# Performance work log

Hardware: AMD Instinct MI355X
Metric: run time of the kernel (lower is better)

Reference implementation:

```python
import jax, jax.numpy as jnp
import numpy as np

D = 128  # h_dim == in_dim

def _gat_layer(h, d, src, dst, n_dst, W, U, V, a):
    # h: [N_src, Din], d: [E, 1], src/dst: [E]
    z = h @ W.T          # [N_src, D]
    zi = h @ U.T         # [N_src, D]
    t = d @ V.T          # [E, 1]
    Dh = W.shape[0]
    # attn_fc on concat([z_src, z_dst, t]) split into three partial dots
    e = z[src] @ a[:Dh] + z[dst] @ a[Dh:2 * Dh] + t[:, 0] * a[2 * Dh]
    e = jax.nn.leaky_relu(e)  # [E]
    # segment softmax over incoming edges of each dst node
    m = jax.ops.segment_max(e, dst, num_segments=n_dst)
    ex = jnp.exp(e - m[dst])
    s = jax.ops.segment_sum(ex, dst, num_segments=n_dst)
    alpha = ex / s[dst]  # [E]
    zn = jax.ops.segment_sum(alpha[:, None] * z[src], dst, num_segments=n_dst)
    return jax.nn.relu(zi[:n_dst] + zn)


def setup_inputs() -> dict:
    key = jax.random.key(0)
    ks = jax.random.split(key, 16)
    N0, ND0, ND1 = 100000, 40000, 20000
    E0, E1 = 640000, 320000
    sc = 1.0 / np.sqrt(D)
    inp = {
        "attr": jax.random.normal(ks[0], (N0, D), jnp.float32),
        "d0": jax.random.normal(ks[1], (E0, 1), jnp.float32),
        "d1": jax.random.normal(ks[2], (E1, 1), jnp.float32),
        "src0": jax.random.randint(ks[3], (E0,), 0, N0, jnp.int32),
        "dst0": jax.random.randint(ks[4], (E0,), 0, ND0, jnp.int32),
        "src1": jax.random.randint(ks[5], (E1,), 0, ND0, jnp.int32),
        "dst1": jax.random.randint(ks[6], (E1,), 0, ND1, jnp.int32),
        "n_dst0": ND0,
        "n_dst1": ND1,
        "W0": jax.random.normal(ks[7], (D, D), jnp.float32) * sc,
        "U0": jax.random.normal(ks[8], (D, D), jnp.float32) * sc,
        "V0": jax.random.normal(ks[9], (1, 1), jnp.float32),
        "a0": jax.random.normal(ks[10], (2 * D + 1,), jnp.float32) * sc,
        "W1": jax.random.normal(ks[11], (D, D), jnp.float32) * sc,
        "U1": jax.random.normal(ks[12], (D, D), jnp.float32) * sc,
        "V1": jax.random.normal(ks[13], (1, 1), jnp.float32),
        "a1": jax.random.normal(ks[14], (2 * D + 1,), jnp.float32) * sc,
    }
    return inp


def reference(attr, d0, d1, W0, U0, V0, a0, W1, U1, V1, a1,
              src0, dst0, src1, dst1, n_dst0, n_dst1):
    h = _gat_layer(attr, d0, src0, dst0, n_dst0, W0, U0, V0, a0)
    h = _gat_layer(h, d1, src1, dst1, n_dst1, W1, U1, V1, a1)
    return h
```

## Files before the change

### kernel.cpp

```cpp
#include <hip/hip_runtime.h>
#include <math.h>


#define D 128

typedef __bf16 bf16x8 __attribute__((ext_vector_type(8)));
typedef float f32x4 __attribute__((ext_vector_type(4)));

static __device__ __forceinline__ float lrelu(float x) {
  return x >= 0.f ? x : 0.01f * x;
}
static __device__ __forceinline__ unsigned short f2bf(float v) {
  unsigned int u = __float_as_uint(v);
  u += 0x7fffu + ((u >> 16) & 1u);
  return (unsigned short)(u >> 16);
}
static __device__ __forceinline__ float bf2f(unsigned short b) {
  return __uint_as_float((unsigned int)b << 16);
}

static __device__ __forceinline__ float4 loadV4(const float* p) {
  return *(const float4*)p;
}
static __device__ __forceinline__ float4 loadV4(const unsigned short* p) {
  ushort4 t = *(const ushort4*)p;
  return make_float4(bf2f(t.x), bf2f(t.y), bf2f(t.z), bf2f(t.w));
}
static __device__ __forceinline__ void storeV4(float* p, float4 v) {
  *(float4*)p = v;
}
static __device__ __forceinline__ void storeV4(unsigned short* p, float4 v) {
  ushort4 t;
  t.x = f2bf(v.x);
  t.y = f2bf(v.y);
  t.z = f2bf(v.z);
  t.w = f2bf(v.w);
  *(ushort4*)p = t;
}
static __device__ __forceinline__ void storeZi(float* p, float v) { *p = v; }
static __device__ __forceinline__ void storeZi(unsigned short* p, float v) {
  *p = f2bf(v);
}

static __device__ __forceinline__ int swz(int row, int colb) {
  return row * 256 + (colb ^ ((row & 7) << 4));
}

__global__ __launch_bounds__(256) void cvt4_kernel(
    const float* __restrict__ s0, const float* __restrict__ s1,
    const float* __restrict__ s2, const float* __restrict__ s3,
    __bf16* __restrict__ dst) {
  int idx = blockIdx.x * 256 + threadIdx.x;
  const float* s = (idx < 16384) ? s0
                   : (idx < 32768) ? s1
                   : (idx < 49152) ? s2 : s3;
  dst[idx] = (__bf16)s[idx & 16383];
}

__global__ void zero_int_kernel(int* __restrict__ p, int n) {
  int i = blockIdx.x * 256 + threadIdx.x;
  if (i < n) p[i] = 0;
}

static __device__ __forceinline__ void stageA(const float* A, int rblk,
                                              int rlim, int t,
                                              unsigned char* ldsA) {
  const char* base = (const char*)A + (size_t)rblk * 512;
#pragma unroll
  for (int g = 0; g < 8; ++g) {
    int sb = g * 4096 + t * 16;
    float4 v = make_float4(0.f, 0.f, 0.f, 0.f);
    if (rblk + (sb >> 9) < rlim) v = *(const float4*)(base + sb);
    int db = sb >> 1;
    int row = db >> 8, colb = db & 255;
    ushort4 o;
    o.x = f2bf(v.x);
    o.y = f2bf(v.y);
    o.z = f2bf(v.z);
    o.w = f2bf(v.w);
    *(ushort4*)(&ldsA[swz(row, colb)]) = o;
  }
}
static __device__ __forceinline__ void stageA(const unsigned short* A,
                                              int rblk, int rlim, int t,
                                              unsigned char* ldsA) {
  const char* base = (const char*)A + (size_t)rblk * 256;
#pragma unroll
  for (int g = 0; g < 4; ++g) {
    int bi = g * 4096 + t * 16;
    int row = bi >> 8, colb = bi & 255;
    ushort4 lo = {0, 0, 0, 0}, hi = {0, 0, 0, 0};
    if (rblk + row < rlim) {
      lo = *(const ushort4*)(base + bi);
      hi = *(const ushort4*)(base + bi + 8);
    }
    *(ushort4*)(&ldsA[swz(row, colb)]) = lo;
    *(ushort4*)(&ldsA[swz(row, colb) + 8]) = hi;
  }
}

template <typename AT, typename ZiT>
__global__ __launch_bounds__(256, 3) void gemm_lds(
    const AT* __restrict__ A, const __bf16* __restrict__ Wb,
    const __bf16* __restrict__ Ub, unsigned short* __restrict__ z,
    ZiT* __restrict__ zi, const float* __restrict__ a,
    float* __restrict__ zs, float* __restrict__ zd, int n_wb, int rows,
    int ndst) {
  __shared__ unsigned char lds[49152];
  const int t = threadIdx.x;
  const int blk = blockIdx.x;
  const bool isU = (blk >= n_wb);
  const int rblk = (isU ? blk - n_wb : blk) * 64;
  const int rlim = isU ? ndst : rows;
  const __bf16* B = isU ? Ub : Wb;

#pragma unroll
  for (int g = 0; g < 8; ++g) {
    int bi = g * 4096 + t * 16;
    int row = bi >> 8, colb = bi & 255;
    bf16x8 v = *(const bf16x8*)((const char*)B + bi);
    *(bf16x8*)(&lds[swz(row, colb)]) = v;
  }
  stageA(A, rblk, rlim, t, lds + 32768);
  __syncthreads();

  const int wave = t >> 6;
  const int lane = t & 63;
  const int lm = lane & 15;
  const int lk = lane >> 4;
  const int r0 = rblk + wave * 16;
  if (r0 >= rlim) return;

  bf16x8 af[4];
#pragma unroll
  for (int kt = 0; kt < 4; ++kt) {
    int row = wave * 16 + lm;
    af[kt] = *(const bf16x8*)(&lds[32768 + swz(row, kt * 64 + lk * 16)]);
  }

  f32x4 acc[8];
#pragma unroll
  for (int tt = 0; tt < 8; ++tt) acc[tt] = (f32x4){0.f, 0.f, 0.f, 0.f};
#pragma unroll
  for (int kt = 0; kt < 4; ++kt) {
#pragma unroll
    for (int tt = 0; tt < 8; ++tt) {
      int row = tt * 16 + lm;
      bf16x8 bf = *(const bf16x8*)(&lds[swz(row, kt * 64 + lk * 16)]);
      acc[tt] =
          __builtin_amdgcn_mfma_f32_16x16x32_bf16(af[kt], bf, acc[tt], 0, 0, 0);
    }
  }

  if (!isU) {
#pragma unroll
    for (int tt = 0; tt < 8; ++tt)
#pragma unroll
      for (int rr = 0; rr < 4; ++rr)
        z[(size_t)(r0 + lk * 4 + rr) * D + tt * 16 + lm] = f2bf(acc[tt][rr]);

    float p1[4] = {0.f, 0.f, 0.f, 0.f};
    float p2[4] = {0.f, 0.f, 0.f, 0.f};
#pragma unroll
    for (int tt = 0; tt < 8; ++tt) {
      float a1 = a[tt * 16 + lm];
      float a2 = a[D + tt * 16 + lm];
#pragma unroll
      for (int rr = 0; rr < 4; ++rr) {
        p1[rr] += acc[tt][rr] * a1;
        p2[rr] += acc[tt][rr] * a2;
      }
    }
#pragma unroll
    for (int rr = 0; rr < 4; ++rr) {
#pragma unroll
      for (int o = 1; o < 16; o <<= 1) {
        p1[rr] += __shfl_xor(p1[rr], o);
        p2[rr] += __shfl_xor(p2[rr], o);
      }
      if (lm == 0) {
        zs[r0 + lk * 4 + rr] = p1[rr];
        zd[r0 + lk * 4 + rr] = p2[rr];
      }
    }
  } else {
#pragma unroll
    for (int tt = 0; tt < 8; ++tt)
#pragma unroll
      for (int rr = 0; rr < 4; ++rr)
        storeZi(&zi[(size_t)(r0 + lk * 4 + rr) * D + tt * 16 + lm],
                acc[tt][rr]);
  }
}

__global__ void count_rank_kernel(const int* __restrict__ dst0,
                                  const int* __restrict__ dst1,
                                  int* __restrict__ cnt0,
                                  int* __restrict__ cnt1,
                                  int* __restrict__ rank0,
                                  int* __restrict__ rank1, int q0, int q1) {
  int gid = blockIdx.x * 256 + threadIdx.x;
  const int* dst;
  int* cnt;
  int* rank;
  int i0;
  if (gid < q0) {
    dst = dst0; cnt = cnt0; rank = rank0; i0 = gid * 4;
  } else if (gid < q0 + q1) {
    dst = dst1; cnt = cnt1; rank = rank1; i0 = (gid - q0) * 4;
  } else {
    return;
  }
  int4 d4 = *(const int4*)(dst + i0);
  int4 r4;
  r4.x = atomicAdd(&cnt[d4.x], 1);
  r4.y = atomicAdd(&cnt[d4.y], 1);
  r4.z = atomicAdd(&cnt[d4.z], 1);
  r4.w = atomicAdd(&cnt[d4.w], 1);
  *(int4*)(rank + i0) = r4;
}

__global__ __launch_bounds__(256) void scan_partial2(
    const int* __restrict__ cnt0, const int* __restrict__ cnt1,
    int* __restrict__ part, int nb0, int n0, int n1) {
  __shared__ int sm[4];
  int blk = blockIdx.x;
  const int* cnt;
  int* pt;
  int n, lb;
  if (blk < nb0) {
    cnt = cnt0; pt = part; n = n0; lb = blk;
  } else {
    cnt = cnt1; pt = part + 64; n = n1; lb = blk - nb0;
  }
  int base = lb * 1024;
  int t = threadIdx.x;
  int s = 0;
#pragma unroll
  for (int i = 0; i < 4; ++i) {
    int idx = base + t + i * 256;
    s += (idx < n) ? cnt[idx] : 0;
  }
  for (int o = 32; o; o >>= 1) s += __shfl_xor(s, o);
  if ((t & 63) == 0) sm[t >> 6] = s;
  __syncthreads();
  if (t == 0) pt[lb] = sm[0] + sm[1] + sm[2] + sm[3];
}

__global__ __launch_bounds__(256) void scan_final2(
    const int* __restrict__ cnt0, const int* __restrict__ cnt1,
    const int* __restrict__ part, int* __restrict__ offs0,
    int* __restrict__ offs1, int nb0, int n0, int n1, int tot0, int tot1) {
  __shared__ int sm[4];
  __shared__ int sbase;
  int blk = blockIdx.x;
  const int* cnt;
  const int* pt;
  int* offs;
  int n, lb, total;
  if (blk < nb0) {
    cnt = cnt0; pt = part; offs = offs0; n = n0; lb = blk; total = tot0;
  } else {
    cnt = cnt1; pt = part + 64; offs = offs1; n = n1; lb = blk - nb0;
    total = tot1;
  }
  int base = lb * 1024;
  int t = threadIdx.x;
  if (t < 64) {
    int v = (t < lb) ? pt[t] : 0;
#pragma unroll
    for (int o = 32; o; o >>= 1) v += __shfl_xor(v, o);
    if (t == 0) sbase = v;
  }
  int idx = base + t * 4;
  int c0 = (idx + 0 < n) ? cnt[idx + 0] : 0;
  int c1 = (idx + 1 < n) ? cnt[idx + 1] : 0;
  int c2 = (idx + 2 < n) ? cnt[idx + 2] : 0;
  int c3 = (idx + 3 < n) ? cnt[idx + 3] : 0;
  int ts = c0 + c1 + c2 + c3;
  int v = ts;
#pragma unroll
  for (int o = 1; o < 64; o <<= 1) {
    int u = __shfl_up(v, o);
    if ((t & 63) >= o) v += u;
  }
  if ((t & 63) == 63) sm[t >> 6] = v;
  __syncthreads();
  int w = t >> 6;
  int waveoff = 0;
  if (w > 0) waveoff += sm[0];
  if (w > 1) waveoff += sm[1];
  if (w > 2) waveoff += sm[2];
  int run = v - ts + waveoff + sbase;
  if (idx + 0 < n) { offs[idx + 0] = run; run += c0; }
  if (idx + 1 < n) { offs[idx + 1] = run; run += c1; }
  if (idx + 2 < n) { offs[idx + 2] = run; run += c2; }
  if (idx + 3 < n) { offs[idx + 3] = run; run += c3; }
  if (lb == 0 && t == 0) offs[n] = total;
}

__global__ void scatter_w_kernel(const int* __restrict__ src,
                                 const int* __restrict__ dst,
                                 const float* __restrict__ dE,
                                 const float* __restrict__ zs,
                                 const float* __restrict__ zd,
                                 const float* __restrict__ V,
                                 const float* __restrict__ a,
                                 const int* __restrict__ rank,
                                 const int* __restrict__ offs,
                                 int2* __restrict__ csr, int E) {
  int i0 = (blockIdx.x * 256 + threadIdx.x) * 4;
  float vc = V[0] * a[2 * D];
  if (i0 + 4 <= E) {
    int4 s4 = *(const int4*)(src + i0);
    int4 d4 = *(const int4*)(dst + i0);
    float4 de = *(const float4*)(dE + i0);
    int4 r4 = *(const int4*)(rank + i0);
    float zs0 = zs[s4.x], zs1 = zs[s4.y], zs2 = zs[s4.z], zs3 = zs[s4.w];
    float zd0 = zd[d4.x], zd1 = zd[d4.y], zd2 = zd[d4.z], zd3 = zd[d4.w];
    int p0 = offs[d4.x] + r4.x;
    int p1 = offs[d4.y] + r4.y;
    int p2 = offs[d4.z] + r4.z;
    int p3 = offs[d4.w] + r4.w;
    float w0 = __expf(lrelu(zs0 + zd0 + de.x * vc));
    float w1 = __expf(lrelu(zs1 + zd1 + de.y * vc));
    float w2 = __expf(lrelu(zs2 + zd2 + de.z * vc));
    float w3 = __expf(lrelu(zs3 + zd3 + de.w * vc));
    csr[p0] = make_int2(s4.x, __float_as_int(w0));
    csr[p1] = make_int2(s4.y, __float_as_int(w1));
    csr[p2] = make_int2(s4.z, __float_as_int(w2));
    csr[p3] = make_int2(s4.w, __float_as_int(w3));
  } else {
    for (int i = i0; i < E; ++i) {
      int di = dst[i];
      int pp = offs[di] + rank[i];
      float w = __expf(lrelu(zs[src[i]] + zd[di] + dE[i] * vc));
      csr[pp] = make_int2(src[i], __float_as_int(w));
    }
  }
}

template <typename OT>
__global__ __launch_bounds__(256) void gat_perdst(
    const unsigned short* __restrict__ z, const int2* __restrict__ csr,
    const int* __restrict__ offs, const OT* __restrict__ ziin,
    OT* __restrict__ hout, int nd) {
  int n = blockIdx.x * 8 + (threadIdx.x >> 5);
  if (n >= nd) return;
  int lane = threadIdx.x & 31;
  int beg = offs[n], end = offs[n + 1];

  float s0 = 0.f, s1 = 0.f;
  float4 acc0 = make_float4(0.f, 0.f, 0.f, 0.f);
  float4 acc1 = make_float4(0.f, 0.f, 0.f, 0.f);
  const unsigned short* zp = z + lane * 4;
  int j = beg;
  for (; j + 8 <= end; j += 8) {
    int2 pr[8];
#pragma unroll
    for (int u = 0; u < 8; ++u) pr[u] = csr[j + u];
    float4 zv[8];
#pragma unroll
    for (int u = 0; u < 8; ++u) zv[u] = loadV4(zp + (size_t)pr[u].x * D);
#pragma unroll
    for (int u = 0; u < 8; u += 2) {
      float wa = __int_as_float(pr[u].y);
      float wb = __int_as_float(pr[u + 1].y);
      s0 += wa;
      acc0.x += wa * zv[u].x;
      acc0.y += wa * zv[u].y;
      acc0.z += wa * zv[u].z;
      acc0.w += wa * zv[u].w;
      s1 += wb;
      acc1.x += wb * zv[u + 1].x;
      acc1.y += wb * zv[u + 1].y;
      acc1.z += wb * zv[u + 1].z;
      acc1.w += wb * zv[u + 1].w;
    }
  }
  for (; j < end; ++j) {
    int2 pr = csr[j];
    float w = __int_as_float(pr.y);
    float4 zv = loadV4(zp + (size_t)pr.x * D);
    s0 += w;
    acc0.x += w * zv.x;
    acc0.y += w * zv.y;
    acc0.z += w * zv.z;
    acc0.w += w * zv.w;
  }
  float s = s0 + s1;
  float inv = (s > 0.f) ? 1.f / s : 0.f;
  float4 acc = make_float4(acc0.x + acc1.x, acc0.y + acc1.y, acc0.z + acc1.z,
                           acc0.w + acc1.w);
  float4 ziv = loadV4(ziin + (size_t)n * D + lane * 4);
  float4 o4;
  o4.x = fmaxf(ziv.x + acc.x * inv, 0.f);
  o4.y = fmaxf(ziv.y + acc.y * inv, 0.f);
  o4.z = fmaxf(ziv.z + acc.z * inv, 0.f);
  o4.w = fmaxf(ziv.w + acc.w * inv, 0.f);
  storeV4(hout + (size_t)n * D + lane * 4, o4);
}

extern "C" void kernel_launch(void* const* d_in, const int* in_sizes, int n_in,
                              void* d_out, int out_size, void* d_ws,
                              size_t ws_size, hipStream_t stream) {
  const float* attr = (const float*)d_in[0];
  const float* d0 = (const float*)d_in[1];
  const float* d1 = (const float*)d_in[2];
  const int* src0 = (const int*)d_in[3];
  const int* dst0 = (const int*)d_in[4];
  const int* src1 = (const int*)d_in[5];
  const int* dst1 = (const int*)d_in[6];
  const float* W0 = (const float*)d_in[9];
  const float* U0 = (const float*)d_in[10];
  const float* V0 = (const float*)d_in[11];
  const float* a0 = (const float*)d_in[12];
  const float* W1 = (const float*)d_in[13];
  const float* U1 = (const float*)d_in[14];
  const float* V1 = (const float*)d_in[15];
  const float* a1 = (const float*)d_in[16];

  const int N0 = in_sizes[0] / D;
  const int E0 = in_sizes[1];
  const int E1 = in_sizes[2];
  const int ND0 = 40000;
  const int ND1 = 20000;

  char* p = (char*)d_ws;
  auto alloc = [&](size_t bytes) {
    char* q = p;
    p += (bytes + 255) & ~(size_t)255;
    return q;
  };
  unsigned short* z = (unsigned short*)alloc((size_t)N0 * D * 2);
  int2* csr = (int2*)alloc((size_t)E0 * 8);
  unsigned short* h1b = (unsigned short*)alloc((size_t)ND0 * D * 2);
  int* rank0 = (int*)alloc((size_t)E0 * 4);
  int* rank1 = (int*)alloc((size_t)E1 * 4);
  float* zs = (float*)alloc((size_t)N0 * 4);
  float* zd = (float*)alloc((size_t)N0 * 4);
  int* offs0 = (int*)alloc((size_t)(ND0 + 1) * 4);
  int* offs1 = (int*)alloc((size_t)(ND1 + 1) * 4);
  int* cnt01 = (int*)alloc((size_t)(ND0 + ND1) * 4);
  int* part = (int*)alloc((size_t)128 * 4);
  __bf16* wb = (__bf16*)alloc((size_t)4 * D * D * 2);
  int* cnt0 = cnt01;
  int* cnt1 = cnt01 + ND0;
  (void)n_in;
  (void)out_size;
  (void)ws_size;

  float* out = (float*)d_out;

  cvt4_kernel<<<256, 256, 0, stream>>>(W0, U0, W1, U1, wb);
  zero_int_kernel<<<(ND0 + ND1 + 255) / 256, 256, 0, stream>>>(cnt01,
                                                               ND0 + ND1);
  {
    int q0 = E0 / 4, q1 = E1 / 4;
    count_rank_kernel<<<(q0 + q1 + 255) / 256, 256, 0, stream>>>(
        dst0, dst1, cnt0, cnt1, rank0, rank1, q0, q1);
    int nb0 = (ND0 + 1023) / 1024;
    int nb1 = (ND1 + 1023) / 1024;
    scan_partial2<<<nb0 + nb1, 256, 0, stream>>>(cnt0, cnt1, part, nb0, ND0,
                                                 ND1);
    scan_final2<<<nb0 + nb1, 256, 0, stream>>>(cnt0, cnt1, part, offs0, offs1,
                                               nb0, ND0, ND1, E0, E1);
  }
  const __bf16* W0b = wb;
  const __bf16* U0b = wb + 16384;
  const __bf16* W1b = wb + 32768;
  const __bf16* U1b = wb + 49152;

  {
    int n_wb = (N0 + 63) / 64, n_ub = (ND0 + 63) / 64;
    gemm_lds<float, unsigned short><<<n_wb + n_ub, 256, 0, stream>>>(
        attr, W0b, U0b, z, (unsigned short*)d_out, a0, zs, zd, n_wb, N0, ND0);
  }
  scatter_w_kernel<<<(E0 / 4 + 255) / 256, 256, 0, stream>>>(
      src0, dst0, d0, zs, zd, V0, a0, rank0, offs0, csr, E0);
  gat_perdst<unsigned short><<<(ND0 + 7) / 8, 256, 0, stream>>>(
      z, csr, offs0, (const unsigned short*)d_out, h1b, ND0);

  {
    int n_wb = (ND0 + 63) / 64, n_ub = (ND1 + 63) / 64;
    gemm_lds<unsigned short, float><<<n_wb + n_ub, 256, 0, stream>>>(
        h1b, W1b, U1b, z, out, a1, zs, zd, n_wb, ND0, ND1);
  }
  scatter_w_kernel<<<(E1 / 4 + 255) / 256, 256, 0, stream>>>(
      src1, dst1, d1, zs, zd, V1, a1, rank1, offs1, csr, E1);
  gat_perdst<float><<<(ND1 + 7) / 8, 256, 0, stream>>>(z, csr, offs1, out, out,
                                                       ND1);
}
```

Measured before the change: 171.3 us.

## Fuse edge count/rank atomics into first GEMM launch via interleaved blocks

Merges the destination-degree counting kernel into the layer-0 GEMM launch. A subset of blocks, interleaved every IL blocks, performs the atomic counting, while the remaining blocks do the GEMM. This removes one kernel launch and lets the latency-bound atomics overlap with the compute-bound GEMM. The cost is an extra branch and larger arguments for the second-layer GEMM, plus possible LDS-driven occupancy interactions, since the count blocks also reserve 48KB of static LDS.

```diff
diff --git a/kernel.cpp b/kernel.cpp
--- a/kernel.cpp
+++ b/kernel.cpp
@@ -100,17 +100,45 @@
 }
 
 template <typename AT, typename ZiT>
-__global__ __launch_bounds__(256, 3) void gemm_lds(
+__global__ __launch_bounds__(256, 3) void gemm_count(
     const AT* __restrict__ A, const __bf16* __restrict__ Wb,
     const __bf16* __restrict__ Ub, unsigned short* __restrict__ z,
     ZiT* __restrict__ zi, const float* __restrict__ a,
     float* __restrict__ zs, float* __restrict__ zd, int n_wb, int rows,
-    int ndst) {
+    int ndst, const int* __restrict__ dst0, const int* __restrict__ dst1,
+    int* __restrict__ cnt0, int* __restrict__ cnt1, int* __restrict__ rank0,
+    int* __restrict__ rank1, int q0, int q1, int IL, int nC) {
   __shared__ unsigned char lds[49152];
+  const int blk = blockIdx.x;
   const int t = threadIdx.x;
-  const int blk = blockIdx.x;
-  const bool isU = (blk >= n_wb);
-  const int rblk = (isU ? blk - n_wb : blk) * 64;
+
+  if ((blk % IL) == 0 && (blk / IL) < nC) {
+    int gid = (blk / IL) * 256 + t;
+    const int* dst;
+    int* cnt;
+    int* rank;
+    int i0;
+    if (gid < q0) {
+      dst = dst0; cnt = cnt0; rank = rank0; i0 = gid * 4;
+    } else if (gid < q0 + q1) {
+      dst = dst1; cnt = cnt1; rank = rank1; i0 = (gid - q0) * 4;
+    } else {
+      return;
+    }
+    int4 d4 = *(const int4*)(dst + i0);
+    int4 r4;
+    r4.x = atomicAdd(&cnt[d4.x], 1);
+    r4.y = atomicAdd(&cnt[d4.y], 1);
+    r4.z = atomicAdd(&cnt[d4.z], 1);
+    r4.w = atomicAdd(&cnt[d4.w], 1);
+    *(int4*)(rank + i0) = r4;
+    return;
+  }
+  const int cb = min(nC, (blk + IL - 1) / IL);
+  const int gb = blk - cb;
+
+  const bool isU = (gb >= n_wb);
+  const int rblk = (isU ? gb - n_wb : gb) * 64;
   const int rlim = isU ? ndst : rows;
   const __bf16* B = isU ? Ub : Wb;
 
@@ -191,33 +219,6 @@
         storeZi(&zi[(size_t)(r0 + lk * 4 + rr) * D + tt * 16 + lm],
                 acc[tt][rr]);
   }
-}
-
-__global__ void count_rank_kernel(const int* __restrict__ dst0,
-                                  const int* __restrict__ dst1,
-                                  int* __restrict__ cnt0,
-                                  int* __restrict__ cnt1,
-                                  int* __restrict__ rank0,
-                                  int* __restrict__ rank1, int q0, int q1) {
-  int gid = blockIdx.x * 256 + threadIdx.x;
-  const int* dst;
-  int* cnt;
-  int* rank;
-  int i0;
-  if (gid < q0) {
-    dst = dst0; cnt = cnt0; rank = rank0; i0 = gid * 4;
-  } else if (gid < q0 + q1) {
-    dst = dst1; cnt = cnt1; rank = rank1; i0 = (gid - q0) * 4;
-  } else {
-    return;
-  }
-  int4 d4 = *(const int4*)(dst + i0);
-  int4 r4;
-  r4.x = atomicAdd(&cnt[d4.x], 1);
-  r4.y = atomicAdd(&cnt[d4.y], 1);
-  r4.z = atomicAdd(&cnt[d4.z], 1);
-  r4.w = atomicAdd(&cnt[d4.w], 1);
-  *(int4*)(rank + i0) = r4;
 }
 
 __global__ __launch_bounds__(256) void scan_partial2(
@@ -455,10 +456,24 @@
   cvt4_kernel<<<256, 256, 0, stream>>>(W0, U0, W1, U1, wb);
   zero_int_kernel<<<(ND0 + ND1 + 255) / 256, 256, 0, stream>>>(cnt01,
                                                                ND0 + ND1);
+  const __bf16* W0b = wb;
+  const __bf16* U0b = wb + 16384;
+  const __bf16* W1b = wb + 32768;
+  const __bf16* U1b = wb + 49152;
+
   {
     int q0 = E0 / 4, q1 = E1 / 4;
-    count_rank_kernel<<<(q0 + q1 + 255) / 256, 256, 0, stream>>>(
-        dst0, dst1, cnt0, cnt1, rank0, rank1, q0, q1);
+    int nC = (q0 + q1 + 255) / 256;
+    int n_wb = (N0 + 63) / 64;
+    int n_ub = (ND0 + 63) / 64;
+    int nG = n_wb + n_ub;
+    int total = nG + nC;
+    int IL = total / nC;
+    gemm_count<float, unsigned short><<<total, 256, 0, stream>>>(
+        attr, W0b, U0b, z, (unsigned short*)d_out, a0, zs, zd, n_wb, N0, ND0,
+        dst0, dst1, cnt0, cnt1, rank0, rank1, q0, q1, IL, nC);
+  }
+  {
     int nb0 = (ND0 + 1023) / 1024;
     int nb1 = (ND1 + 1023) / 1024;
     scan_partial2<<<nb0 + nb1, 256, 0, stream>>>(cnt0, cnt1, part, nb0, ND0,
@@ -466,16 +481,6 @@
     scan_final2<<<nb0 + nb1, 256, 0, stream>>>(cnt0, cnt1, part, offs0, offs1,
                                                nb0, ND0, ND1, E0, E1);
   }
-  const __bf16* W0b = wb;
-  const __bf16* U0b = wb + 16384;
-  const __bf16* W1b = wb + 32768;
-  const __bf16* U1b = wb + 49152;
-
-  {
-    int n_wb = (N0 + 63) / 64, n_ub = (ND0 + 63) / 64;
-    gemm_lds<float, unsigned short><<<n_wb + n_ub, 256, 0, stream>>>(
-        attr, W0b, U0b, z, (unsigned short*)d_out, a0, zs, zd, n_wb, N0, ND0);
-  }
   scatter_w_kernel<<<(E0 / 4 + 255) / 256, 256, 0, stream>>>(
       src0, dst0, d0, zs, zd, V0, a0, rank0, offs0, csr, E0);
   gat_perdst<unsigned short><<<(ND0 + 7) / 8, 256, 0, stream>>>(
@@ -483,8 +488,9 @@
 
   {
     int n_wb = (ND0 + 63) / 64, n_ub = (ND1 + 63) / 64;
-    gemm_lds<unsigned short, float><<<n_wb + n_ub, 256, 0, stream>>>(
-        h1b, W1b, U1b, z, out, a1, zs, zd, n_wb, ND0, ND1);
+    gemm_count<unsigned short, float><<<n_wb + n_ub, 256, 0, stream>>>(
+        h1b, W1b, U1b, z, out, a1, zs, zd, n_wb, ND0, ND1, nullptr, nullptr,
+        nullptr, nullptr, nullptr, nullptr, 0, 0, 1, 0);
   }
   scatter_w_kernel<<<(E1 / 4 + 255) / 256, 256, 0, stream>>>(
       src1, dst1, d1, zs, zd, V1, a1, rank1, offs1, csr, E1);
```

Measured after the change: 154.3 us. -9.9%, faster.
